# Performance work log

Hardware: AMD Instinct MI355X
Metric: run time of the kernel (lower is better)

## Reference

```python
import jax, jax.numpy as jnp
import numpy as np

ATOM_FDIM = 35
BOND_FDIM = 5
MAX_NB = 10
HIDDEN = 128
DEPTH = 6
N_ATOMS = 100000
N_BONDS = 220000
N_MESS = 20000
N_MOLS = 2000


def setup_inputs() -> dict:
    key = jax.random.key(0)
    ks = jax.random.split(key, 10)
    fatoms = jax.random.uniform(ks[0], (N_ATOMS, ATOM_FDIM), dtype=jnp.float32)
    fbonds = jax.random.uniform(ks[1], (N_BONDS, ATOM_FDIM + BOND_FDIM), dtype=jnp.float32)
    tree_message = jax.random.normal(ks[2], (N_MESS, HIDDEN), dtype=jnp.float32)
    tree_message = tree_message.at[0].set(0.0)  # index 0 is the zero-padding message
    agraph = jax.random.randint(ks[3], (N_ATOMS, MAX_NB), 0, N_MESS + N_BONDS, dtype=jnp.int32)
    bgraph = jax.random.randint(ks[4], (N_BONDS, MAX_NB), 0, N_MESS + N_BONDS, dtype=jnp.int32)
    mol_ids = jnp.sort(jax.random.randint(ks[5], (N_ATOMS,), 0, N_MOLS, dtype=jnp.int32))
    # learned parameters (torch Linear stores W as [out, in]; we keep [in, out])
    def lin(k, fan_in, fan_out):
        bound = 1.0 / np.sqrt(fan_in)
        return jax.random.uniform(k, (fan_in, fan_out), minval=-bound, maxval=bound, dtype=jnp.float32)
    W_i = lin(ks[6], ATOM_FDIM + BOND_FDIM, HIDDEN)
    W_h = lin(ks[7], HIDDEN, HIDDEN)
    W_o = lin(ks[8], ATOM_FDIM + HIDDEN, HIDDEN)
    b_o = jax.random.uniform(ks[9], (HIDDEN,), minval=-1.0 / np.sqrt(ATOM_FDIM + HIDDEN), maxval=1.0 / np.sqrt(ATOM_FDIM + HIDDEN), dtype=jnp.float32)
    return {
        'fatoms': fatoms, 'fbonds': fbonds, 'tree_message': tree_message,
        'agraph': agraph, 'bgraph': bgraph, 'mol_ids': mol_ids, 'n_mols': N_MOLS,
        'W_i': W_i, 'W_h': W_h, 'W_o': W_o, 'b_o': b_o,
    }


def reference(fatoms, fbonds, tree_message, agraph, bgraph, mol_ids, n_mols, W_i, W_h, W_o, b_o):
    binput = fbonds @ W_i                    # [B, H]
    graph_message = jax.nn.relu(binput)
    for _ in range(DEPTH - 1):
        message = jnp.concatenate([tree_message, graph_message], axis=0)  # [M+B, H]
        nei = message[bgraph].sum(axis=1)    # gather [B, MAX_NB, H] -> sum -> [B, H]
        graph_message = jax.nn.relu(binput + nei @ W_h)
    message = jnp.concatenate([tree_message, graph_message], axis=0)
    nei_a = message[agraph].sum(axis=1)      # [A, H]
    ainput = jnp.concatenate([fatoms, nei_a], axis=1)  # [A, ATOM_FDIM+H]
    atom_hiddens = jax.nn.relu(ainput @ W_o + b_o)     # [A, H]
    # mean-pool per molecule (scope)
    sums = jax.ops.segment_sum(atom_hiddens, mol_ids, num_segments=n_mols)
    counts = jax.ops.segment_sum(jnp.ones((atom_hiddens.shape[0],), dtype=atom_hiddens.dtype), mol_ids, num_segments=n_mols)
    mol_vecs = sums / jnp.maximum(counts, 1.0)[:, None]
    return mol_vecs
```

## Files before the change

kernel.cpp:

```cpp
#include <hip/hip_runtime.h>

#define N_ATOMS   100000
#define N_BONDS   220000
#define N_MESS    20000
#define N_MSG     (N_MESS + N_BONDS)
#define ATOM_FDIM 35
#define BOND_FDIM 5
#define BOND_IN   (ATOM_FDIM + BOND_FDIM)
#define H         128
#define MAX_NB    10
#define NB_PAD    12
#define DEPTH     6
#define KO        (ATOM_FDIM + H)
#define KC        192
#define QLDS_STR  144
#define SC_BIAS   887u

typedef __attribute__((ext_vector_type(8))) short short8;
typedef __attribute__((ext_vector_type(4))) float f32x4;

static __device__ __forceinline__ float asf(unsigned int u) {
    union { unsigned int i; float f; } v; v.i = u; return v.f;
}

static __device__ __forceinline__ unsigned short f2bf(float f) {
    union { float f; unsigned int i; } v; v.f = f;
    unsigned int x = v.i;
    return (unsigned short)((x + 0x7FFFu + ((x >> 16) & 1u)) >> 16);
}

static __device__ __forceinline__ float ub2f(unsigned int v, int b) {
    return (float)((v >> (b * 8)) & 0xffu);
}

static __device__ __forceinline__ int sc_code(float mx) {
    float t = mx * (1.f / 127.f);
    int code = (int)((__float_as_uint(t) + 0xFFFFFu) >> 20) - (int)SC_BIAS;
    return code < 1 ? 1 : (code > 255 ? 255 : code);
}
static __device__ __forceinline__ float sc_val(int code) {
    return asf(((unsigned)code + SC_BIAS) << 20);
}

#define PTa (N_BONDS * BOND_IN)
#define PTb (PTa + H * KC)
#define PTc (PTb + H * KC)
#define PTd (PTc + N_BONDS * MAX_NB)
#define PTe (PTd + N_ATOMS * MAX_NB)

__global__ __launch_bounds__(256) void prep(
    const float* __restrict__ fbonds,
    const float* __restrict__ Wi, const float* __restrict__ Wh,
    const float* __restrict__ Wo,
    const int* __restrict__ bgraph, const int* __restrict__ agraph,
    ushort* __restrict__ fbc, ushort* __restrict__ WT,
    ushort* __restrict__ WoT,
    int* __restrict__ bgP, int* __restrict__ agP,
    float* __restrict__ out, int n_out)
{
    int i = blockIdx.x * 256 + threadIdx.x;
    if (i < PTa) {
        fbc[i] = f2bf(fbonds[i]);
    } else if (i < PTb) {
        int j = i - PTa;
        int n = j / KC, k = j - n * KC;
        float v = (k < BOND_IN) ? Wi[k * H + n]
                : (k < BOND_IN + H) ? Wh[(k - BOND_IN) * H + n] : 0.f;
        WT[j] = f2bf(v);
    } else if (i < PTc) {
        int j = i - PTb;
        int n = j / KC, k = j - n * KC;
        float v = (k < H) ? Wo[(ATOM_FDIM + k) * H + n]
                : (k < KO) ? Wo[(k - H) * H + n] : 0.f;
        WoT[j] = f2bf(v);
    } else if (i < PTd) {
        int j = i - PTc;
        int b = j / MAX_NB, n = j - b * MAX_NB;
        bgP[b * NB_PAD + n] = bgraph[j];
    } else if (i < PTe) {
        int j = i - PTd;
        int a = j / MAX_NB, n = j - a * MAX_NB;
        agP[a * NB_PAD + n] = agraph[j];
    } else {
        int j = i - PTe;
        if (j < n_out) out[j] = 0.f;
    }
}

__global__ __launch_bounds__(256) void qtree(
    const float* __restrict__ tree,
    ushort* __restrict__ qA, ushort* __restrict__ qB,
    unsigned char* __restrict__ sA, unsigned char* __restrict__ sB)
{
    int row = blockIdx.x * 4 + (threadIdx.x >> 6);
    int lane = threadIdx.x & 63;
    float2 v = *(const float2*)&tree[(size_t)row * H + lane * 2];
    float mx = fmaxf(fabsf(v.x), fabsf(v.y));
    #pragma unroll
    for (int d = 1; d <= 32; d <<= 1)
        mx = fmaxf(mx, __shfl_xor(mx, d));
    int code = sc_code(mx);
    float inv = __builtin_amdgcn_rcpf(sc_val(code));
    int u0 = __float2int_rn(v.x * inv) + 128;
    int u1 = __float2int_rn(v.y * inv) + 128;
    u0 = u0 < 0 ? 0 : (u0 > 255 ? 255 : u0);
    u1 = u1 < 0 ? 0 : (u1 > 255 ? 255 : u1);
    unsigned short pk = (unsigned short)(u0 | (u1 << 8));
    qA[(size_t)row * 64 + lane] = pk;
    qB[(size_t)row * 64 + lane] = pk;
    if (lane == 0) { sA[row] = (unsigned char)code; sB[row] = (unsigned char)code; }
}

static __device__ __forceinline__ uint4 gather_u8c(
    const uint2* __restrict__ msgq, const unsigned char* __restrict__ scl,
    const int* __restrict__ gidx, int c16)
{
    uint4 i0 = *(const uint4*)gidx;
    uint4 i1 = *(const uint4*)(gidx + 4);
    uint2 i2 = *(const uint2*)(gidx + 8);
    int idx[MAX_NB] = {(int)i0.x, (int)i0.y, (int)i0.z, (int)i0.w,
                       (int)i1.x, (int)i1.y, (int)i1.z, (int)i1.w,
                       (int)i2.x, (int)i2.y};
    float scf[MAX_NB];
    uint2 d[MAX_NB];
    #pragma unroll
    for (int n = 0; n < MAX_NB; n++) {
        scf[n] = sc_val((int)scl[idx[n]]);
        d[n] = msgq[(size_t)idx[n] * 16 + c16];
    }
    float s0=0.f,s1=0.f,s2=0.f,s3=0.f,s4=0.f,s5=0.f,s6=0.f,s7=0.f;
    float ssum = 0.f;
    #pragma unroll
    for (int n = 0; n < MAX_NB; n++) {
        float sc = scf[n]; ssum += sc;
        s0 += sc * ub2f(d[n].x, 0); s1 += sc * ub2f(d[n].x, 1);
        s2 += sc * ub2f(d[n].x, 2); s3 += sc * ub2f(d[n].x, 3);
        s4 += sc * ub2f(d[n].y, 0); s5 += sc * ub2f(d[n].y, 1);
        s6 += sc * ub2f(d[n].y, 2); s7 += sc * ub2f(d[n].y, 3);
    }
    s0 = fmaf(-128.f, ssum, s0); s1 = fmaf(-128.f, ssum, s1);
    s2 = fmaf(-128.f, ssum, s2); s3 = fmaf(-128.f, ssum, s3);
    s4 = fmaf(-128.f, ssum, s4); s5 = fmaf(-128.f, ssum, s5);
    s6 = fmaf(-128.f, ssum, s6); s7 = fmaf(-128.f, ssum, s7);
    uint4 pk;
    asm("v_cvt_pk_bf16_f32 %0, %1, %2" : "=v"(pk.x) : "v"(s0), "v"(s1));
    asm("v_cvt_pk_bf16_f32 %0, %1, %2" : "=v"(pk.y) : "v"(s2), "v"(s3));
    asm("v_cvt_pk_bf16_f32 %0, %1, %2" : "=v"(pk.z) : "v"(s4), "v"(s5));
    asm("v_cvt_pk_bf16_f32 %0, %1, %2" : "=v"(pk.w) : "v"(s6), "v"(s7));
    return pk;
}

static __device__ __forceinline__ void u8_epilogue(
    f32x4 c00, f32x4 c01, f32x4 c10, f32x4 c11,
    int tid, int row_base,
    float* rmx , float* qp , char* qlds,
    uint4* __restrict__ gq4, unsigned char* __restrict__ scout)
{
    int lane = tid & 63, wv = tid >> 6;
    int m_lane = lane & 15, quad = lane >> 4;
    int n0 = wv * 32;

    float v00[4], v01[4], v10[4], v11[4];
    #pragma unroll
    for (int r = 0; r < 4; r++) {
        v00[r] = fmaxf(c00[r], 0.f); v01[r] = fmaxf(c01[r], 0.f);
        v10[r] = fmaxf(c10[r], 0.f); v11[r] = fmaxf(c11[r], 0.f);
    }
    #pragma unroll
    for (int r = 0; r < 4; r++) {
        float mx0 = fmaxf(v00[r], v01[r]);
        float mx1 = fmaxf(v10[r], v11[r]);
        #pragma unroll
        for (int d = 1; d <= 8; d <<= 1) {
            mx0 = fmaxf(mx0, __shfl_xor(mx0, d));
            mx1 = fmaxf(mx1, __shfl_xor(mx1, d));
        }
        if (m_lane == 0) {
            rmx[(quad * 4 + r) * 4 + wv]      = mx0;
            rmx[(quad * 4 + r + 16) * 4 + wv] = mx1;
        }
    }
    __syncthreads();
    if (tid < 32) {
        float mx = fmaxf(fmaxf(rmx[tid * 4], rmx[tid * 4 + 1]),
                         fmaxf(rmx[tid * 4 + 2], rmx[tid * 4 + 3]));
        int code = sc_code(mx);
        qp[tid] = __builtin_amdgcn_rcpf(sc_val(code));
        scout[row_base + tid] = (unsigned char)code;
    }
    __syncthreads();
    #pragma unroll
    for (int r = 0; r < 4; r++) {
        int r0 = quad * 4 + r, r1 = r0 + 16;
        float i0 = qp[r0], i1 = qp[r1];
        int u00 = __float2int_rn(v00[r] * i0) + 128;
        int u01 = __float2int_rn(v01[r] * i0) + 128;
        int u10 = __float2int_rn(v10[r] * i1) + 128;
        int u11 = __float2int_rn(v11[r] * i1) + 128;
        qlds[r0 * QLDS_STR + n0 + m_lane]      = (char)(u00 > 255 ? 255 : u00);
        qlds[r0 * QLDS_STR + n0 + 16 + m_lane] = (char)(u01 > 255 ? 255 : u01);
        qlds[r1 * QLDS_STR + n0 + m_lane]      = (char)(u10 > 255 ? 255 : u10);
        qlds[r1 * QLDS_STR + n0 + 16 + m_lane] = (char)(u11 > 255 ? 255 : u11);
    }
    __syncthreads();
    int row = tid >> 3, seg = tid & 7;
    uint4 w = *(const uint4*)(qlds + row * QLDS_STR + seg * 16);
    gq4[(size_t)(row_base + row) * 8 + seg] = w;
}

__global__ __launch_bounds__(256, 4) void binput0(
    const ushort* __restrict__ fbc, const ushort* __restrict__ WT,
    uint4* __restrict__ gq_out, unsigned char* __restrict__ sc_out)
{
    __shared__ ushort Xlds[32 * 25 * 8];
    __shared__ __align__(16) char qlds[32 * QLDS_STR];
    __shared__ float rmx[32 * 4];
    __shared__ float qp[32];

    int tid = threadIdx.x;
    int bond0 = blockIdx.x * 32;
    int lane = tid & 63, wv = tid >> 6;

    if (tid < 160) {
        int b = tid / 5, k8 = tid - b * 5;
        *(short8*)&Xlds[(b * 25 + k8) * 8] =
            *(const short8*)&fbc[(size_t)bond0 * BOND_IN + tid * 8];
    }
    if (tid < 96) {
        int b = tid / 3, k8 = 5 + (tid - b * 3);
        *(float4*)&Xlds[(b * 25 + k8) * 8] = float4{0.f, 0.f, 0.f, 0.f};
    }
    __syncthreads();

    int n0 = wv * 32;
    int m_lane = lane & 15, quad = lane >> 4;
    f32x4 c00 = {0,0,0,0}, c01 = {0,0,0,0}, c10 = {0,0,0,0}, c11 = {0,0,0,0};

    #pragma unroll
    for (int s = 0; s < 2; s++) {
        short8 a0 = *(const short8*)&Xlds[((m_lane)      * 25 + s * 4 + quad) * 8];
        short8 a1 = *(const short8*)&Xlds[((16 + m_lane) * 25 + s * 4 + quad) * 8];
        short8 b0 = *(const short8*)&WT[(size_t)(n0 + m_lane)      * KC + s * 32 + quad * 8];
        short8 b1 = *(const short8*)&WT[(size_t)(n0 + 16 + m_lane) * KC + s * 32 + quad * 8];
        c00 = __builtin_amdgcn_mfma_f32_16x16x32_bf16(a0, b0, c00, 0, 0, 0);
        c01 = __builtin_amdgcn_mfma_f32_16x16x32_bf16(a0, b1, c01, 0, 0, 0);
        c10 = __builtin_amdgcn_mfma_f32_16x16x32_bf16(a1, b0, c10, 0, 0, 0);
        c11 = __builtin_amdgcn_mfma_f32_16x16x32_bf16(a1, b1, c11, 0, 0, 0);
    }

    u8_epilogue(c00, c01, c10, c11, tid, bond0, rmx, qp, qlds, gq_out, sc_out);
}

__global__ __launch_bounds__(256, 4) void mp_round(
    const uint2* __restrict__ msg_in, const unsigned char* __restrict__ sc_in,
    const ushort* __restrict__ fbc, const int* __restrict__ bgraphP,
    const ushort* __restrict__ WT,
    uint4* __restrict__ gq_out, unsigned char* __restrict__ sc_out)
{
    __shared__ ushort Xlds[32 * 25 * 8];
    __shared__ __align__(16) char qlds[32 * QLDS_STR];
    __shared__ float rmx[32 * 4];
    __shared__ float qp[32];

    int tid = threadIdx.x;
    int bond0 = blockIdx.x * 32;
    int lane = tid & 63, wv = tid >> 6;
    int q = lane >> 4, c16 = lane & 15;

    if (tid < 160) {
        int b = tid / 5, k8 = tid - b * 5;
        *(short8*)&Xlds[(b * 25 + k8) * 8] =
            *(const short8*)&fbc[(size_t)bond0 * BOND_IN + tid * 8];
    }
    if (tid < 96) {
        int b = tid / 3, k8 = 21 + (tid - b * 3);
        *(float4*)&Xlds[(b * 25 + k8) * 8] = float4{0.f, 0.f, 0.f, 0.f};
    }
    #pragma unroll
    for (int g = 0; g < 2; g++) {
        int b = wv + 4 * (g * 4 + q);
        uint4 pk = gather_u8c(msg_in, sc_in,
                              bgraphP + (size_t)(bond0 + b) * NB_PAD, c16);
        *(uint4*)&Xlds[(b * 25 + 5 + c16) * 8] = pk;
    }
    __syncthreads();

    int n0 = wv * 32;
    int m_lane = lane & 15, quad = lane >> 4;
    f32x4 c00 = {0,0,0,0}, c01 = {0,0,0,0}, c10 = {0,0,0,0}, c11 = {0,0,0,0};

    #pragma unroll
    for (int s = 0; s < KC / 32; s++) {
        short8 a0 = *(const short8*)&Xlds[((m_lane)      * 25 + s * 4 + quad) * 8];
        short8 a1 = *(const short8*)&Xlds[((16 + m_lane) * 25 + s * 4 + quad) * 8];
        short8 b0 = *(const short8*)&WT[(size_t)(n0 + m_lane)      * KC + s * 32 + quad * 8];
        short8 b1 = *(const short8*)&WT[(size_t)(n0 + 16 + m_lane) * KC + s * 32 + quad * 8];
        c00 = __builtin_amdgcn_mfma_f32_16x16x32_bf16(a0, b0, c00, 0, 0, 0);
        c01 = __builtin_amdgcn_mfma_f32_16x16x32_bf16(a0, b1, c01, 0, 0, 0);
        c10 = __builtin_amdgcn_mfma_f32_16x16x32_bf16(a1, b0, c10, 0, 0, 0);
        c11 = __builtin_amdgcn_mfma_f32_16x16x32_bf16(a1, b1, c11, 0, 0, 0);
    }

    u8_epilogue(c00, c01, c10, c11, tid, bond0, rmx, qp, qlds, gq_out, sc_out);
}

__global__ __launch_bounds__(256, 4) void atom_mfma(
    const float* __restrict__ fatoms, const uint2* __restrict__ msg,
    const unsigned char* __restrict__ scl,
    const int* __restrict__ agraphP, const ushort* __restrict__ WoT,
    const float* __restrict__ bo, const int* __restrict__ mol_ids,
    float* __restrict__ out)
{
    __shared__ ushort Xlds[32 * 25 * 8];
    __shared__ float htile[32 * H];
    __shared__ int mlds[32];

    int tid = threadIdx.x;
    int a0 = blockIdx.x * 32;
    int lane = tid & 63, wv = tid >> 6;
    int q = lane >> 4, c16 = lane & 15;

    for (int i = tid; i < 32 * ATOM_FDIM; i += 256) {
        int b = i / ATOM_FDIM, t = i - b * ATOM_FDIM;
        int k = H + t;
        Xlds[(b * 25 + (k >> 3)) * 8 + (k & 7)] = f2bf(fatoms[(size_t)a0 * ATOM_FDIM + i]);
    }
    if (tid < 160) {
        int b = tid / 5, k = 163 + (tid - b * 5);
        Xlds[(b * 25 + (k >> 3)) * 8 + (k & 7)] = 0;
    }
    if (tid < 96) {
        int b = tid / 3, k8 = 21 + (tid - b * 3);
        *(float4*)&Xlds[(b * 25 + k8) * 8] = float4{0.f, 0.f, 0.f, 0.f};
    }
    if (tid < 32) mlds[tid] = mol_ids[a0 + tid];
    #pragma unroll
    for (int g = 0; g < 2; g++) {
        int b = wv + 4 * (g * 4 + q);
        uint4 pk = gather_u8c(msg, scl,
                              agraphP + (size_t)(a0 + b) * NB_PAD, c16);
        *(uint4*)&Xlds[(b * 25 + c16) * 8] = pk;
    }
    __syncthreads();

    int n0 = wv * 32;
    int m_lane = lane & 15, quad = lane >> 4;
    float bias0 = bo[n0 + m_lane], bias1 = bo[n0 + 16 + m_lane];
    f32x4 c00 = {bias0, bias0, bias0, bias0};
    f32x4 c01 = {bias1, bias1, bias1, bias1};
    f32x4 c10 = {bias0, bias0, bias0, bias0};
    f32x4 c11 = {bias1, bias1, bias1, bias1};

    #pragma unroll
    for (int s = 0; s < KC / 32; s++) {
        short8 a0f = *(const short8*)&Xlds[((m_lane)      * 25 + s * 4 + quad) * 8];
        short8 a1f = *(const short8*)&Xlds[((16 + m_lane) * 25 + s * 4 + quad) * 8];
        short8 b0f = *(const short8*)&WoT[(size_t)(n0 + m_lane)      * KC + s * 32 + quad * 8];
        short8 b1f = *(const short8*)&WoT[(size_t)(n0 + 16 + m_lane) * KC + s * 32 + quad * 8];
        c00 = __builtin_amdgcn_mfma_f32_16x16x32_bf16(a0f, b0f, c00, 0, 0, 0);
        c01 = __builtin_amdgcn_mfma_f32_16x16x32_bf16(a0f, b1f, c01, 0, 0, 0);
        c10 = __builtin_amdgcn_mfma_f32_16x16x32_bf16(a1f, b0f, c10, 0, 0, 0);
        c11 = __builtin_amdgcn_mfma_f32_16x16x32_bf16(a1f, b1f, c11, 0, 0, 0);
    }

    #pragma unroll
    for (int r = 0; r < 4; r++) {
        int r0 = quad * 4 + r, r1 = r0 + 16;
        htile[r0 * H + n0 + m_lane]      = fmaxf(c00[r], 0.f);
        htile[r0 * H + n0 + 16 + m_lane] = fmaxf(c01[r], 0.f);
        htile[r1 * H + n0 + m_lane]      = fmaxf(c10[r], 0.f);
        htile[r1 * H + n0 + 16 + m_lane] = fmaxf(c11[r], 0.f);
    }
    __syncthreads();

    if (tid < H) {
        int j = tid;
        float acc = 0.f;
        int cur = mlds[0];
        for (int r = 0; r < 32; r++) {
            int m = mlds[r];
            if (m != cur) {
                atomicAdd(&out[(size_t)cur * H + j], acc);
                acc = 0.f; cur = m;
            }
            acc += htile[r * H + j];
        }
        atomicAdd(&out[(size_t)cur * H + j], acc);
    }
}

__global__ __launch_bounds__(128) void pool_div(
    const int* __restrict__ mol_ids, float* __restrict__ out, int n_atoms)
{
    int m = blockIdx.x;
    int j = threadIdx.x;

    int lo = 0, hi = n_atoms;
    while (lo < hi) { int mid = (lo + hi) >> 1; if (mol_ids[mid] < m) lo = mid + 1; else hi = mid; }
    int start = lo;
    hi = n_atoms;
    while (lo < hi) { int mid = (lo + hi) >> 1; if (mol_ids[mid] < m + 1) lo = mid + 1; else hi = mid; }
    int end = lo;

    out[(size_t)m * H + j] /= fmaxf((float)(end - start), 1.f);
}

extern "C" void kernel_launch(void* const* d_in, const int* in_sizes, int n_in,
                              void* d_out, int out_size, void* d_ws, size_t ws_size,
                              hipStream_t stream)
{
    const float* fatoms  = (const float*)d_in[0];
    const float* fbonds  = (const float*)d_in[1];
    const float* tree    = (const float*)d_in[2];
    const int*   agraph  = (const int*)d_in[3];
    const int*   bgraph  = (const int*)d_in[4];
    const int*   mol_ids = (const int*)d_in[5];
    const float* W_i = (const float*)d_in[7];
    const float* W_h = (const float*)d_in[8];
    const float* W_o = (const float*)d_in[9];
    const float* b_o = (const float*)d_in[10];
    float* out = (float*)d_out;

    uint2* mqA = (uint2*)d_ws;
    uint2* mqB = mqA + (size_t)N_MSG * 16;
    unsigned char* scA = (unsigned char*)(mqB + (size_t)N_MSG * 16);
    unsigned char* scB = scA + N_MSG;
    ushort* WT  = (ushort*)(scB + N_MSG);
    ushort* WoT = WT + (size_t)H * KC;
    ushort* fbc = WoT + (size_t)H * KC;
    int* bgP = (int*)(fbc + (size_t)N_BONDS * BOND_IN);
    int* agP = bgP + (size_t)N_BONDS * NB_PAD;

    int prep_total = PTe + out_size;
    prep<<<(prep_total + 255) / 256, 256, 0, stream>>>(
        fbonds, W_i, W_h, W_o, bgraph, agraph, fbc, WT, WoT, bgP, agP, out, out_size);

    qtree<<<N_MESS / 4, 256, 0, stream>>>(tree, (ushort*)mqA, (ushort*)mqB, scA, scB);

    binput0<<<N_BONDS / 32, 256, 0, stream>>>(fbc, WT,
        (uint4*)(mqA + (size_t)N_MESS * 16), scA + N_MESS);

    const uint2* tin = mqA; const unsigned char* sin = scA;
    uint2* tout = mqB; unsigned char* sout = scB;
    for (int r = 0; r < DEPTH - 1; r++) {
        mp_round<<<N_BONDS / 32, 256, 0, stream>>>(tin, sin, fbc, bgP, WT,
            (uint4*)(tout + (size_t)N_MESS * 16), sout + N_MESS);
        const uint2* t1 = tin; tin = tout; tout = (uint2*)t1;
        const unsigned char* t2 = sin; sin = sout; sout = (unsigned char*)t2;
    }

    atom_mfma<<<N_ATOMS / 32, 256, 0, stream>>>(fatoms, tin, sin, agP, WoT, b_o,
                                                mol_ids, out);

    int n_mols = out_size / H;
    pool_div<<<n_mols, 128, 0, stream>>>(mol_ids, out, N_ATOMS);
}
```

Measured before the change: 546.0 us.

## Fuse prep/qtree/count kernels, fold mean division into atomics, batch gathers, alias LDS

Merges the tree quantisation and per-molecule inverse-count computation into the prep kernel as extra block ranges, and removes the separate pool_div kernel by scaling each atomic add by the precomputed inverse count. The neighbour gather now issues loads for two bonds' indices before decoding either, which raises memory-level parallelism at some register cost. The quantisation staging buffer is aliased onto the X tile in shared memory to cut LDS use per block. Together these remove two launches and are meant to improve gather latency hiding and occupancy.

Measured after the change: 547.1 us. Within noise of the previous version (+0.2%).

```diff
diff --git a/kernel.cpp b/kernel.cpp
--- a/kernel.cpp
+++ b/kernel.cpp
@@ -47,92 +47,92 @@
 #define PTc (PTb + H * KC)
 #define PTd (PTc + N_BONDS * MAX_NB)
 #define PTe (PTd + N_ATOMS * MAX_NB)
+#define NB_QT (N_MESS / 4)
 
 __global__ __launch_bounds__(256) void prep(
     const float* __restrict__ fbonds,
     const float* __restrict__ Wi, const float* __restrict__ Wh,
     const float* __restrict__ Wo,
     const int* __restrict__ bgraph, const int* __restrict__ agraph,
+    const float* __restrict__ tree, const int* __restrict__ mol_ids,
     ushort* __restrict__ fbc, ushort* __restrict__ WT,
     ushort* __restrict__ WoT,
     int* __restrict__ bgP, int* __restrict__ agP,
-    float* __restrict__ out, int n_out)
-{
-    int i = blockIdx.x * 256 + threadIdx.x;
-    if (i < PTa) {
-        fbc[i] = f2bf(fbonds[i]);
-    } else if (i < PTb) {
-        int j = i - PTa;
-        int n = j / KC, k = j - n * KC;
-        float v = (k < BOND_IN) ? Wi[k * H + n]
-                : (k < BOND_IN + H) ? Wh[(k - BOND_IN) * H + n] : 0.f;
-        WT[j] = f2bf(v);
-    } else if (i < PTc) {
-        int j = i - PTb;
-        int n = j / KC, k = j - n * KC;
-        float v = (k < H) ? Wo[(ATOM_FDIM + k) * H + n]
-                : (k < KO) ? Wo[(k - H) * H + n] : 0.f;
-        WoT[j] = f2bf(v);
-    } else if (i < PTd) {
-        int j = i - PTc;
-        int b = j / MAX_NB, n = j - b * MAX_NB;
-        bgP[b * NB_PAD + n] = bgraph[j];
-    } else if (i < PTe) {
-        int j = i - PTd;
-        int a = j / MAX_NB, n = j - a * MAX_NB;
-        agP[a * NB_PAD + n] = agraph[j];
+    ushort* __restrict__ qA, ushort* __restrict__ qB,
+    unsigned char* __restrict__ sA, unsigned char* __restrict__ sB,
+    float* __restrict__ icnt,
+    float* __restrict__ out, int n_out, int nbElem, int n_mols)
+{
+    int blk = blockIdx.x;
+    int tid = threadIdx.x;
+
+    if (blk < nbElem) {
+        int i = blk * 256 + tid;
+        if (i < PTa) {
+            fbc[i] = f2bf(fbonds[i]);
+        } else if (i < PTb) {
+            int j = i - PTa;
+            int n = j / KC, k = j - n * KC;
+            float v = (k < BOND_IN) ? Wi[k * H + n]
+                    : (k < BOND_IN + H) ? Wh[(k - BOND_IN) * H + n] : 0.f;
+            WT[j] = f2bf(v);
+        } else if (i < PTc) {
+            int j = i - PTb;
+            int n = j / KC, k = j - n * KC;
+            float v = (k < H) ? Wo[(ATOM_FDIM + k) * H + n]
+                    : (k < KO) ? Wo[(k - H) * H + n] : 0.f;
+            WoT[j] = f2bf(v);
+        } else if (i < PTd) {
+            int j = i - PTc;
+            int b = j / MAX_NB, n = j - b * MAX_NB;
+            bgP[b * NB_PAD + n] = bgraph[j];
+        } else if (i < PTe) {
+            int j = i - PTd;
+            int a = j / MAX_NB, n = j - a * MAX_NB;
+            agP[a * NB_PAD + n] = agraph[j];
+        } else {
+            int j = i - PTe;
+            if (j < n_out) out[j] = 0.f;
+        }
+    } else if (blk < nbElem + NB_QT) {
+        int row = (blk - nbElem) * 4 + (tid >> 6);
+        int lane = tid & 63;
+        float2 v = *(const float2*)&tree[(size_t)row * H + lane * 2];
+        float mx = fmaxf(fabsf(v.x), fabsf(v.y));
+        #pragma unroll
+        for (int d = 1; d <= 32; d <<= 1)
+            mx = fmaxf(mx, __shfl_xor(mx, d));
+        int code = sc_code(mx);
+        float inv = __builtin_amdgcn_rcpf(sc_val(code));
+        int u0 = __float2int_rn(v.x * inv) + 128;
+        int u1 = __float2int_rn(v.y * inv) + 128;
+        u0 = u0 < 0 ? 0 : (u0 > 255 ? 255 : u0);
+        u1 = u1 < 0 ? 0 : (u1 > 255 ? 255 : u1);
+        unsigned short pk = (unsigned short)(u0 | (u1 << 8));
+        qA[(size_t)row * 64 + lane] = pk;
+        qB[(size_t)row * 64 + lane] = pk;
+        if (lane == 0) { sA[row] = (unsigned char)code; sB[row] = (unsigned char)code; }
     } else {
-        int j = i - PTe;
-        if (j < n_out) out[j] = 0.f;
-    }
-}
-
-__global__ __launch_bounds__(256) void qtree(
-    const float* __restrict__ tree,
-    ushort* __restrict__ qA, ushort* __restrict__ qB,
-    unsigned char* __restrict__ sA, unsigned char* __restrict__ sB)
-{
-    int row = blockIdx.x * 4 + (threadIdx.x >> 6);
-    int lane = threadIdx.x & 63;
-    float2 v = *(const float2*)&tree[(size_t)row * H + lane * 2];
-    float mx = fmaxf(fabsf(v.x), fabsf(v.y));
-    #pragma unroll
-    for (int d = 1; d <= 32; d <<= 1)
-        mx = fmaxf(mx, __shfl_xor(mx, d));
-    int code = sc_code(mx);
-    float inv = __builtin_amdgcn_rcpf(sc_val(code));
-    int u0 = __float2int_rn(v.x * inv) + 128;
-    int u1 = __float2int_rn(v.y * inv) + 128;
-    u0 = u0 < 0 ? 0 : (u0 > 255 ? 255 : u0);
-    u1 = u1 < 0 ? 0 : (u1 > 255 ? 255 : u1);
-    unsigned short pk = (unsigned short)(u0 | (u1 << 8));
-    qA[(size_t)row * 64 + lane] = pk;
-    qB[(size_t)row * 64 + lane] = pk;
-    if (lane == 0) { sA[row] = (unsigned char)code; sB[row] = (unsigned char)code; }
-}
-
-static __device__ __forceinline__ uint4 gather_u8c(
-    const uint2* __restrict__ msgq, const unsigned char* __restrict__ scl,
-    const int* __restrict__ gidx, int c16)
-{
-    uint4 i0 = *(const uint4*)gidx;
-    uint4 i1 = *(const uint4*)(gidx + 4);
-    uint2 i2 = *(const uint2*)(gidx + 8);
-    int idx[MAX_NB] = {(int)i0.x, (int)i0.y, (int)i0.z, (int)i0.w,
-                       (int)i1.x, (int)i1.y, (int)i1.z, (int)i1.w,
-                       (int)i2.x, (int)i2.y};
-    float scf[MAX_NB];
-    uint2 d[MAX_NB];
-    #pragma unroll
-    for (int n = 0; n < MAX_NB; n++) {
-        scf[n] = sc_val((int)scl[idx[n]]);
-        d[n] = msgq[(size_t)idx[n] * 16 + c16];
-    }
+        int m = (blk - nbElem - NB_QT) * 256 + tid;
+        if (m < n_mols) {
+            int lo = 0, hi = N_ATOMS;
+            while (lo < hi) { int mid = (lo + hi) >> 1; if (mol_ids[mid] < m) lo = mid + 1; else hi = mid; }
+            int start = lo;
+            hi = N_ATOMS;
+            while (lo < hi) { int mid = (lo + hi) >> 1; if (mol_ids[mid] < m + 1) lo = mid + 1; else hi = mid; }
+            icnt[m] = 1.f / fmaxf((float)(lo - start), 1.f);
+        }
+    }
+}
+
+static __device__ __forceinline__ uint4 decode10(
+    const uint2* d, const unsigned char* k)
+{
     float s0=0.f,s1=0.f,s2=0.f,s3=0.f,s4=0.f,s5=0.f,s6=0.f,s7=0.f;
     float ssum = 0.f;
     #pragma unroll
     for (int n = 0; n < MAX_NB; n++) {
-        float sc = scf[n]; ssum += sc;
+        float sc = sc_val((int)k[n]); ssum += sc;
         s0 += sc * ub2f(d[n].x, 0); s1 += sc * ub2f(d[n].x, 1);
         s2 += sc * ub2f(d[n].x, 2); s3 += sc * ub2f(d[n].x, 3);
         s4 += sc * ub2f(d[n].y, 0); s5 += sc * ub2f(d[n].y, 1);
@@ -148,6 +148,33 @@
     asm("v_cvt_pk_bf16_f32 %0, %1, %2" : "=v"(pk.z) : "v"(s4), "v"(s5));
     asm("v_cvt_pk_bf16_f32 %0, %1, %2" : "=v"(pk.w) : "v"(s6), "v"(s7));
     return pk;
+}
+
+static __device__ __forceinline__ void gather2_u8c(
+    const uint2* __restrict__ msgq, const unsigned char* __restrict__ scl,
+    const int* __restrict__ g0, const int* __restrict__ g1, int c16,
+    uint4* pk0, uint4* pk1)
+{
+    uint4 x0 = *(const uint4*)g0; uint4 x1 = *(const uint4*)(g0 + 4);
+    uint2 x2 = *(const uint2*)(g0 + 8);
+    uint4 y0 = *(const uint4*)g1; uint4 y1 = *(const uint4*)(g1 + 4);
+    uint2 y2 = *(const uint2*)(g1 + 8);
+    int ia[MAX_NB] = {(int)x0.x,(int)x0.y,(int)x0.z,(int)x0.w,
+                      (int)x1.x,(int)x1.y,(int)x1.z,(int)x1.w,(int)x2.x,(int)x2.y};
+    int ib[MAX_NB] = {(int)y0.x,(int)y0.y,(int)y0.z,(int)y0.w,
+                      (int)y1.x,(int)y1.y,(int)y1.z,(int)y1.w,(int)y2.x,(int)y2.y};
+    uint2 da[MAX_NB], db[MAX_NB];
+    unsigned char ka[MAX_NB], kb[MAX_NB];
+    #pragma unroll
+    for (int n = 0; n < MAX_NB; n++) da[n] = msgq[(size_t)ia[n] * 16 + c16];
+    #pragma unroll
+    for (int n = 0; n < MAX_NB; n++) db[n] = msgq[(size_t)ib[n] * 16 + c16];
+    #pragma unroll
+    for (int n = 0; n < MAX_NB; n++) ka[n] = scl[ia[n]];
+    #pragma unroll
+    for (int n = 0; n < MAX_NB; n++) kb[n] = scl[ib[n]];
+    *pk0 = decode10(da, ka);
+    *pk1 = decode10(db, kb);
 }
 
 static __device__ __forceinline__ void u8_epilogue(
@@ -212,10 +239,10 @@
     const ushort* __restrict__ fbc, const ushort* __restrict__ WT,
     uint4* __restrict__ gq_out, unsigned char* __restrict__ sc_out)
 {
-    __shared__ ushort Xlds[32 * 25 * 8];
-    __shared__ __align__(16) char qlds[32 * QLDS_STR];
+    __shared__ __align__(16) ushort Xlds[32 * 25 * 8];
     __shared__ float rmx[32 * 4];
     __shared__ float qp[32];
+    char* qlds = (char*)Xlds;
 
     int tid = threadIdx.x;
     int bond0 = blockIdx.x * 32;
@@ -257,10 +284,10 @@
     const ushort* __restrict__ WT,
     uint4* __restrict__ gq_out, unsigned char* __restrict__ sc_out)
 {
-    __shared__ ushort Xlds[32 * 25 * 8];
-    __shared__ __align__(16) char qlds[32 * QLDS_STR];
+    __shared__ __align__(16) ushort Xlds[32 * 25 * 8];
     __shared__ float rmx[32 * 4];
     __shared__ float qp[32];
+    char* qlds = (char*)Xlds;
 
     int tid = threadIdx.x;
     int bond0 = blockIdx.x * 32;
@@ -276,12 +303,14 @@
         int b = tid / 3, k8 = 21 + (tid - b * 3);
         *(float4*)&Xlds[(b * 25 + k8) * 8] = float4{0.f, 0.f, 0.f, 0.f};
     }
-    #pragma unroll
-    for (int g = 0; g < 2; g++) {
-        int b = wv + 4 * (g * 4 + q);
-        uint4 pk = gather_u8c(msg_in, sc_in,
-                              bgraphP + (size_t)(bond0 + b) * NB_PAD, c16);
-        *(uint4*)&Xlds[(b * 25 + 5 + c16) * 8] = pk;
+    {
+        int b0 = wv + 4 * q, b1 = wv + 16 + 4 * q;
+        uint4 pk0, pk1;
+        gather2_u8c(msg_in, sc_in,
+                    bgraphP + (size_t)(bond0 + b0) * NB_PAD,
+                    bgraphP + (size_t)(bond0 + b1) * NB_PAD, c16, &pk0, &pk1);
+        *(uint4*)&Xlds[(b0 * 25 + 5 + c16) * 8] = pk0;
+        *(uint4*)&Xlds[(b1 * 25 + 5 + c16) * 8] = pk1;
     }
     __syncthreads();
 
@@ -309,6 +338,7 @@
     const unsigned char* __restrict__ scl,
     const int* __restrict__ agraphP, const ushort* __restrict__ WoT,
     const float* __restrict__ bo, const int* __restrict__ mol_ids,
+    const float* __restrict__ icnt,
     float* __restrict__ out)
 {
     __shared__ ushort Xlds[32 * 25 * 8];
@@ -334,12 +364,14 @@
         *(float4*)&Xlds[(b * 25 + k8) * 8] = float4{0.f, 0.f, 0.f, 0.f};
     }
     if (tid < 32) mlds[tid] = mol_ids[a0 + tid];
-    #pragma unroll
-    for (int g = 0; g < 2; g++) {
-        int b = wv + 4 * (g * 4 + q);
-        uint4 pk = gather_u8c(msg, scl,
-                              agraphP + (size_t)(a0 + b) * NB_PAD, c16);
-        *(uint4*)&Xlds[(b * 25 + c16) * 8] = pk;
+    {
+        int b0 = wv + 4 * q, b1 = wv + 16 + 4 * q;
+        uint4 pk0, pk1;
+        gather2_u8c(msg, scl,
+                    agraphP + (size_t)(a0 + b0) * NB_PAD,
+                    agraphP + (size_t)(a0 + b1) * NB_PAD, c16, &pk0, &pk1);
+        *(uint4*)&Xlds[(b0 * 25 + c16) * 8] = pk0;
+        *(uint4*)&Xlds[(b1 * 25 + c16) * 8] = pk1;
     }
     __syncthreads();
 
@@ -380,29 +412,13 @@
         for (int r = 0; r < 32; r++) {
             int m = mlds[r];
             if (m != cur) {
-                atomicAdd(&out[(size_t)cur * H + j], acc);
+                atomicAdd(&out[(size_t)cur * H + j], acc * icnt[cur]);
                 acc = 0.f; cur = m;
             }
             acc += htile[r * H + j];
         }
-        atomicAdd(&out[(size_t)cur * H + j], acc);
-    }
-}
-
-__global__ __launch_bounds__(128) void pool_div(
-    const int* __restrict__ mol_ids, float* __restrict__ out, int n_atoms)
-{
-    int m = blockIdx.x;
-    int j = threadIdx.x;
-
-    int lo = 0, hi = n_atoms;
-    while (lo < hi) { int mid = (lo + hi) >> 1; if (mol_ids[mid] < m) lo = mid + 1; else hi = mid; }
-    int start = lo;
-    hi = n_atoms;
-    while (lo < hi) { int mid = (lo + hi) >> 1; if (mol_ids[mid] < m + 1) lo = mid + 1; else hi = mid; }
-    int end = lo;
-
-    out[(size_t)m * H + j] /= fmaxf((float)(end - start), 1.f);
+        atomicAdd(&out[(size_t)cur * H + j], acc * icnt[cur]);
+    }
 }
 
 extern "C" void kernel_launch(void* const* d_in, const int* in_sizes, int n_in,
@@ -425,17 +441,20 @@
     uint2* mqB = mqA + (size_t)N_MSG * 16;
     unsigned char* scA = (unsigned char*)(mqB + (size_t)N_MSG * 16);
     unsigned char* scB = scA + N_MSG;
-    ushort* WT  = (ushort*)(scB + N_MSG);
+    float* icnt = (float*)(scB + N_MSG);
+    ushort* WT  = (ushort*)(icnt + 2048);
     ushort* WoT = WT + (size_t)H * KC;
     ushort* fbc = WoT + (size_t)H * KC;
     int* bgP = (int*)(fbc + (size_t)N_BONDS * BOND_IN);
     int* agP = bgP + (size_t)N_BONDS * NB_PAD;
 
-    int prep_total = PTe + out_size;
-    prep<<<(prep_total + 255) / 256, 256, 0, stream>>>(
-        fbonds, W_i, W_h, W_o, bgraph, agraph, fbc, WT, WoT, bgP, agP, out, out_size);
-
-    qtree<<<N_MESS / 4, 256, 0, stream>>>(tree, (ushort*)mqA, (ushort*)mqB, scA, scB);
+    int n_mols = out_size / H;
+    int nbElem = (PTe + out_size + 255) / 256;
+    int nbTot = nbElem + NB_QT + (n_mols + 255) / 256;
+    prep<<<nbTot, 256, 0, stream>>>(
+        fbonds, W_i, W_h, W_o, bgraph, agraph, tree, mol_ids,
+        fbc, WT, WoT, bgP, agP,
+        (ushort*)mqA, (ushort*)mqB, scA, scB, icnt, out, out_size, nbElem, n_mols);
 
     binput0<<<N_BONDS / 32, 256, 0, stream>>>(fbc, WT,
         (uint4*)(mqA + (size_t)N_MESS * 16), scA + N_MESS);
@@ -450,8 +469,5 @@
     }
 
     atom_mfma<<<N_ATOMS / 32, 256, 0, stream>>>(fatoms, tin, sin, agP, WoT, b_o,
-                                                mol_ids, out);
-
-    int n_mols = out_size / H;
-    pool_div<<<n_mols, 128, 0, stream>>>(mol_ids, out, N_ATOMS);
-}
+                                                mol_ids, icnt, out);
+}
```
